# Kernel optimization log

Hardware: AMD Instinct MI355X
Metric: run time of the kernel (lower is better)

## Reference

```python
import jax, jax.numpy as jnp
import numpy as np

B, N, F_IN, F_OUT = 16, 1024, 128, 128
LEAKY_SLOPE = 0.01  # torch nn.LeakyReLU default


def setup_inputs() -> dict:
    key = jax.random.key(0)
    k1, k2, k3, k4 = jax.random.split(key, 4)
    node_mat = jax.random.normal(k1, (B, N, F_IN), dtype=jnp.float32)
    adj_mat = jax.random.uniform(k2, (B, N, N), dtype=jnp.float32)
    # nn.Linear(node_in_len, node_out_len): weight [F_OUT, F_IN], bias [F_OUT]
    bound = 1.0 / np.sqrt(F_IN)
    W = jax.random.uniform(k3, (F_OUT, F_IN), minval=-bound, maxval=bound, dtype=jnp.float32)
    b = jax.random.uniform(k4, (F_OUT,), minval=-bound, maxval=bound, dtype=jnp.float32)
    return {"node_mat": node_mat, "adj_mat": adj_mat, "W": W, "b": b}


def reference(node_mat, adj_mat, W, b):
    # degree normalization: row-scale adjacency by 1/degree
    # (the torch code builds a diagonal inv-degree matrix and bmm's it;
    #  mathematically identical to a broadcast row scale)
    n_neighbors = adj_mat.sum(axis=-1, keepdims=True)          # [B, N, 1]
    norm_adj = adj_mat / n_neighbors                           # [B, N, N]
    node_fea = jnp.einsum('bnm,bmf->bnf', norm_adj, node_mat)  # [B, N, F_in]
    node_fea = jnp.einsum('bnf,of->bno', node_fea, W) + b      # linear
    return jnp.where(node_fea >= 0, node_fea, LEAKY_SLOPE * node_fea)
```

## Files before the change

kernel.cpp:

```cpp
#include <hip/hip_runtime.h>
#include <hip/hip_bf16.h>


typedef __attribute__((ext_vector_type(8))) __bf16 bf16x8;
typedef __attribute__((ext_vector_type(4))) float f32x4;

__device__ __forceinline__ unsigned f2bf_pk(float lo, float hi) {
    union { float f; unsigned u; } a, b;
    a.f = lo; b.f = hi;
    unsigned ra = (a.u + 0x7FFFu + ((a.u >> 16) & 1u)) >> 16;
    unsigned rb = (b.u + 0x7FFFu + ((b.u >> 16) & 1u)) & 0xFFFF0000u;
    return ra | rb;
}

__device__ __forceinline__ bf16x8 cvt8(const f32x4& a, const f32x4& b) {
    union { unsigned u[4]; bf16x8 v; } r;
    r.u[0] = f2bf_pk(a.x, a.y);
    r.u[1] = f2bf_pk(a.z, a.w);
    r.u[2] = f2bf_pk(b.x, b.y);
    r.u[3] = f2bf_pk(b.z, b.w);
    return r.v;
}

__global__ __launch_bounds__(256, 2)
void k1_xw(const float* __restrict__ x, const float* __restrict__ W,
           unsigned short* __restrict__ yF)
{
    __shared__ unsigned short Ax[64 * 128];
    __shared__ unsigned short Bw[128 * 128];

    const int t   = threadIdx.x;
    const int bid = blockIdx.x;
    const int xcd = bid & 7;
    const int j   = bid >> 3;
    const int b   = xcd * 2 + (j >> 4);
    const int m0  = (j & 15) << 6;
    const float* xb = x + (((long)b << 10) + m0) * 128;

#pragma unroll
    for (int i = 0; i < 8; ++i) {
        int e = i * 1024 + t * 4;
        int r = e >> 7, f = e & 127;
        f32x4 v = *(const f32x4*)(xb + (long)r * 128 + f);
        int c = f >> 3;
        int byte = r * 256 + (((c ^ (r & 7)) << 4) | ((f & 7) << 1));
        uint2 pk; pk.x = f2bf_pk(v.x, v.y); pk.y = f2bf_pk(v.z, v.w);
        *(uint2*)((char*)Ax + byte) = pk;
    }
#pragma unroll
    for (int i = 0; i < 16; ++i) {
        int e = i * 1024 + t * 4;
        int r = e >> 7, f = e & 127;
        f32x4 v = *(const f32x4*)(W + r * 128 + f);
        int c = f >> 3;
        int byte = r * 256 + (((c ^ (r & 7)) << 4) | ((f & 7) << 1));
        uint2 pk; pk.x = f2bf_pk(v.x, v.y); pk.y = f2bf_pk(v.z, v.w);
        *(uint2*)((char*)Bw + byte) = pk;
    }
    __syncthreads();

    const int lane = t & 63, w = t >> 6;
    const int lrow = lane & 15, lq = lane >> 4;

    bf16x8 af[4];
#pragma unroll
    for (int kk = 0; kk < 4; ++kk) {
        int r = w * 16 + lrow;
        int c = kk * 4 + lq;
        af[kk] = *(const bf16x8*)((const char*)Ax + r * 256 + ((c ^ (r & 7)) << 4));
    }

    f32x4 zero = {0.f, 0.f, 0.f, 0.f};
    f32x4 acc[8] = {zero, zero, zero, zero, zero, zero, zero, zero};
#pragma unroll
    for (int nf = 0; nf < 8; ++nf) {
#pragma unroll
        for (int kk = 0; kk < 4; ++kk) {
            int o = nf * 16 + lrow;
            int c = kk * 4 + lq;
            bf16x8 bfrag = *(const bf16x8*)((const char*)Bw + o * 256 + ((c ^ (o & 7)) << 4));
            acc[nf] = __builtin_amdgcn_mfma_f32_16x16x32_bf16(af[kk], bfrag, acc[nf], 0, 0, 0);
        }
    }

    {
        const int ks = (m0 >> 5) + (w >> 1);
        const int q  = (w & 1) * 2 + (lq >> 1);
        const int jb = (lq & 1) * 4;
#pragma unroll
        for (int nf = 0; nf < 8; ++nf) {
            uint2 pk;
            pk.x = f2bf_pk(acc[nf][0], acc[nf][1]);
            pk.y = f2bf_pk(acc[nf][2], acc[nf][3]);
            long off = (((long)((b * 32 + ks) * 8 + nf)) << 9) + (q * 16 + lrow) * 8 + jb;
            *(uint2*)(yF + off) = pk;
        }
    }
}

__global__ __launch_bounds__(256, 1)
void k2_agg(const float* __restrict__ adj, const unsigned short* __restrict__ yF,
            const float* __restrict__ bias, float* __restrict__ out)
{
    __shared__ float accbuf[4][128 * 68];
    __shared__ float degw[4][64];

    const int bid = blockIdx.x;
    const int xcd = bid & 7;
    const int j   = bid >> 3;
    const int b   = xcd * 2 + (j >> 4);
    const int n0  = (j & 15) << 6;

    const int t = threadIdx.x;
    const int lane = t & 63, w = t >> 6;
    const int lrow = lane & 15, lq = lane >> 4;

    const float* adjr = adj + ((long)(b * 1024 + n0 + lrow)) * 1024 + (w << 8) + lq * 8;
    const unsigned short* fr = yF + (((long)(b * 32 + w * 8) * 8) << 9) + lane * 8;

    f32x4 zero = {0.f, 0.f, 0.f, 0.f};
    f32x4 acc[4][8];
#pragma unroll
    for (int rg = 0; rg < 4; ++rg)
#pragma unroll
        for (int ot = 0; ot < 8; ++ot) acc[rg][ot] = zero;
    float ds[4] = {0.f, 0.f, 0.f, 0.f};

#pragma unroll 2
    for (int kk = 0; kk < 8; ++kk) {
        f32x4 v0[4], v1[4];
#pragma unroll
        for (int rg = 0; rg < 4; ++rg) {
            v0[rg] = *(const f32x4*)(adjr + rg * 16384 + kk * 32);
            v1[rg] = *(const f32x4*)(adjr + rg * 16384 + kk * 32 + 4);
        }
        bf16x8 bb[8];
#pragma unroll
        for (int ot = 0; ot < 8; ++ot)
            bb[ot] = *(const bf16x8*)(fr + ((kk * 8 + ot) << 9));

        bf16x8 a[4];
#pragma unroll
        for (int rg = 0; rg < 4; ++rg) {
            ds[rg] += v0[rg].x + v0[rg].y + v0[rg].z + v0[rg].w
                    + v1[rg].x + v1[rg].y + v1[rg].z + v1[rg].w;
            a[rg] = cvt8(v0[rg], v1[rg]);
        }
#pragma unroll
        for (int rg = 0; rg < 4; ++rg)
#pragma unroll
            for (int ot = 0; ot < 8; ++ot)
                acc[rg][ot] = __builtin_amdgcn_mfma_f32_16x16x32_bf16(a[rg], bb[ot], acc[rg][ot], 0, 0, 0);
    }

#pragma unroll
    for (int rg = 0; rg < 4; ++rg) {
        float d = ds[rg];
        d += __shfl_xor(d, 16, 64);
        d += __shfl_xor(d, 32, 64);
        if (lq == 0) degw[w][rg * 16 + lrow] = d;
    }

#pragma unroll
    for (int rg = 0; rg < 4; ++rg)
#pragma unroll
        for (int ot = 0; ot < 8; ++ot)
            *(f32x4*)&accbuf[w][(ot * 16 + lrow) * 68 + rg * 16 + lq * 4] = acc[rg][ot];
    __syncthreads();

    {
        const int n = lane;
        const int o0 = w * 32;
        float deg = degw[0][n] + degw[1][n] + degw[2][n] + degw[3][n];
        float inv = 1.0f / deg;
        float res[32];
#pragma unroll
        for (int c = 0; c < 32; ++c) {
            float s = accbuf[0][(o0 + c) * 68 + n] + accbuf[1][(o0 + c) * 68 + n]
                    + accbuf[2][(o0 + c) * 68 + n] + accbuf[3][(o0 + c) * 68 + n];
            float v = s * inv + bias[o0 + c];
            res[c] = (v >= 0.f) ? v : 0.01f * v;
        }
        float* op = out + (((long)(b * 1024 + n0 + n)) << 7) + o0;
#pragma unroll
        for (int g = 0; g < 8; ++g) {
            f32x4 r = {res[g * 4], res[g * 4 + 1], res[g * 4 + 2], res[g * 4 + 3]};
            *(f32x4*)(op + g * 4) = r;
        }
    }
}

extern "C" void kernel_launch(void* const* d_in, const int* in_sizes, int n_in,
                              void* d_out, int out_size, void* d_ws, size_t ws_size,
                              hipStream_t stream) {
    const float* node = (const float*)d_in[0];
    const float* adj  = (const float*)d_in[1];
    const float* W    = (const float*)d_in[2];
    const float* bias = (const float*)d_in[3];
    float* out = (float*)d_out;
    unsigned short* yF = (unsigned short*)d_ws;

    k1_xw<<<dim3(256), dim3(256), 0, stream>>>(node, W, yF);
    k2_agg<<<dim3(256), dim3(256), 0, stream>>>(adj, yF, bias, out);
}
```

Measured before the change: 27.87 us.

## Split work finer: 32-row tiles in xW kernel, 8 waves per aggregation block

The X·W kernel now uses 32-row tiles across 512 blocks, with each wave computing half the output columns. The aggregation kernel runs 512 threads (8 waves), and each wave handles 32 rows instead of 64. This halves the per-wave accumulator count and raises occupancy and latency hiding on the adjacency stream. The cost is more redundant loads of W per block in k1, a dropped XCD-aware block mapping in k1, and a larger LDS footprint per block under launch_bounds(512,2).

```diff
diff --git a/kernel.cpp b/kernel.cpp
--- a/kernel.cpp
+++ b/kernel.cpp
@@ -26,19 +26,17 @@
 void k1_xw(const float* __restrict__ x, const float* __restrict__ W,
            unsigned short* __restrict__ yF)
 {
-    __shared__ unsigned short Ax[64 * 128];
+    __shared__ unsigned short Ax[32 * 128];
     __shared__ unsigned short Bw[128 * 128];
 
-    const int t   = threadIdx.x;
-    const int bid = blockIdx.x;
-    const int xcd = bid & 7;
-    const int j   = bid >> 3;
-    const int b   = xcd * 2 + (j >> 4);
-    const int m0  = (j & 15) << 6;
+    const int t  = threadIdx.x;
+    const int wg = blockIdx.x;
+    const int b  = wg >> 5;
+    const int m0 = (wg & 31) << 5;
     const float* xb = x + (((long)b << 10) + m0) * 128;
 
 #pragma unroll
-    for (int i = 0; i < 8; ++i) {
+    for (int i = 0; i < 4; ++i) {
         int e = i * 1024 + t * 4;
         int r = e >> 7, f = e & 127;
         f32x4 v = *(const f32x4*)(xb + (long)r * 128 + f);
@@ -60,23 +58,24 @@
     __syncthreads();
 
     const int lane = t & 63, w = t >> 6;
+    const int wm = w >> 1, wn = w & 1;
     const int lrow = lane & 15, lq = lane >> 4;
 
     bf16x8 af[4];
 #pragma unroll
     for (int kk = 0; kk < 4; ++kk) {
-        int r = w * 16 + lrow;
+        int r = wm * 16 + lrow;
         int c = kk * 4 + lq;
         af[kk] = *(const bf16x8*)((const char*)Ax + r * 256 + ((c ^ (r & 7)) << 4));
     }
 
     f32x4 zero = {0.f, 0.f, 0.f, 0.f};
-    f32x4 acc[8] = {zero, zero, zero, zero, zero, zero, zero, zero};
-#pragma unroll
-    for (int nf = 0; nf < 8; ++nf) {
+    f32x4 acc[4] = {zero, zero, zero, zero};
+#pragma unroll
+    for (int nf = 0; nf < 4; ++nf) {
 #pragma unroll
         for (int kk = 0; kk < 4; ++kk) {
-            int o = nf * 16 + lrow;
+            int o = wn * 64 + nf * 16 + lrow;
             int c = kk * 4 + lq;
             bf16x8 bfrag = *(const bf16x8*)((const char*)Bw + o * 256 + ((c ^ (o & 7)) << 4));
             acc[nf] = __builtin_amdgcn_mfma_f32_16x16x32_bf16(af[kk], bfrag, acc[nf], 0, 0, 0);
@@ -84,21 +83,22 @@
     }
 
     {
-        const int ks = (m0 >> 5) + (w >> 1);
-        const int q  = (w & 1) * 2 + (lq >> 1);
+        const int ks = wg & 31;
+        const int q  = wm * 2 + (lq >> 1);
         const int jb = (lq & 1) * 4;
 #pragma unroll
-        for (int nf = 0; nf < 8; ++nf) {
+        for (int nf = 0; nf < 4; ++nf) {
+            int ot = wn * 4 + nf;
             uint2 pk;
             pk.x = f2bf_pk(acc[nf][0], acc[nf][1]);
             pk.y = f2bf_pk(acc[nf][2], acc[nf][3]);
-            long off = (((long)((b * 32 + ks) * 8 + nf)) << 9) + (q * 16 + lrow) * 8 + jb;
+            long off = (((long)((b * 32 + ks) * 8 + ot)) << 9) + (q * 16 + lrow) * 8 + jb;
             *(uint2*)(yF + off) = pk;
         }
     }
 }
 
-__global__ __launch_bounds__(256, 1)
+__global__ __launch_bounds__(512, 2)
 void k2_agg(const float* __restrict__ adj, const unsigned short* __restrict__ yF,
             const float* __restrict__ bias, float* __restrict__ out)
 {
@@ -113,24 +113,25 @@
 
     const int t = threadIdx.x;
     const int lane = t & 63, w = t >> 6;
+    const int h = w >> 2, q = w & 3;
     const int lrow = lane & 15, lq = lane >> 4;
 
-    const float* adjr = adj + ((long)(b * 1024 + n0 + lrow)) * 1024 + (w << 8) + lq * 8;
-    const unsigned short* fr = yF + (((long)(b * 32 + w * 8) * 8) << 9) + lane * 8;
+    const float* adjr = adj + ((long)(b * 1024 + n0 + h * 32 + lrow)) * 1024 + (q << 8) + lq * 8;
+    const unsigned short* fr = yF + (((long)((b * 32 + q * 8) * 8)) << 9) + lane * 8;
 
     f32x4 zero = {0.f, 0.f, 0.f, 0.f};
-    f32x4 acc[4][8];
-#pragma unroll
-    for (int rg = 0; rg < 4; ++rg)
+    f32x4 acc[2][8];
+#pragma unroll
+    for (int rg = 0; rg < 2; ++rg)
 #pragma unroll
         for (int ot = 0; ot < 8; ++ot) acc[rg][ot] = zero;
-    float ds[4] = {0.f, 0.f, 0.f, 0.f};
-
-#pragma unroll 2
+    float ds[2] = {0.f, 0.f};
+
+#pragma unroll
     for (int kk = 0; kk < 8; ++kk) {
-        f32x4 v0[4], v1[4];
-#pragma unroll
-        for (int rg = 0; rg < 4; ++rg) {
+        f32x4 v0[2], v1[2];
+#pragma unroll
+        for (int rg = 0; rg < 2; ++rg) {
             v0[rg] = *(const f32x4*)(adjr + rg * 16384 + kk * 32);
             v1[rg] = *(const f32x4*)(adjr + rg * 16384 + kk * 32 + 4);
         }
@@ -139,43 +140,43 @@
         for (int ot = 0; ot < 8; ++ot)
             bb[ot] = *(const bf16x8*)(fr + ((kk * 8 + ot) << 9));
 
-        bf16x8 a[4];
-#pragma unroll
-        for (int rg = 0; rg < 4; ++rg) {
+        bf16x8 a[2];
+#pragma unroll
+        for (int rg = 0; rg < 2; ++rg) {
             ds[rg] += v0[rg].x + v0[rg].y + v0[rg].z + v0[rg].w
                     + v1[rg].x + v1[rg].y + v1[rg].z + v1[rg].w;
             a[rg] = cvt8(v0[rg], v1[rg]);
         }
 #pragma unroll
-        for (int rg = 0; rg < 4; ++rg)
+        for (int rg = 0; rg < 2; ++rg)
 #pragma unroll
             for (int ot = 0; ot < 8; ++ot)
                 acc[rg][ot] = __builtin_amdgcn_mfma_f32_16x16x32_bf16(a[rg], bb[ot], acc[rg][ot], 0, 0, 0);
     }
 
 #pragma unroll
-    for (int rg = 0; rg < 4; ++rg) {
+    for (int rg = 0; rg < 2; ++rg) {
         float d = ds[rg];
         d += __shfl_xor(d, 16, 64);
         d += __shfl_xor(d, 32, 64);
-        if (lq == 0) degw[w][rg * 16 + lrow] = d;
-    }
-
-#pragma unroll
-    for (int rg = 0; rg < 4; ++rg)
+        if (lq == 0) degw[q][h * 32 + rg * 16 + lrow] = d;
+    }
+
+#pragma unroll
+    for (int rg = 0; rg < 2; ++rg)
 #pragma unroll
         for (int ot = 0; ot < 8; ++ot)
-            *(f32x4*)&accbuf[w][(ot * 16 + lrow) * 68 + rg * 16 + lq * 4] = acc[rg][ot];
+            *(f32x4*)&accbuf[q][(ot * 16 + lrow) * 68 + h * 32 + rg * 16 + lq * 4] = acc[rg][ot];
     __syncthreads();
 
     {
         const int n = lane;
-        const int o0 = w * 32;
+        const int o0 = w * 16;
         float deg = degw[0][n] + degw[1][n] + degw[2][n] + degw[3][n];
         float inv = 1.0f / deg;
-        float res[32];
-#pragma unroll
-        for (int c = 0; c < 32; ++c) {
+        float res[16];
+#pragma unroll
+        for (int c = 0; c < 16; ++c) {
             float s = accbuf[0][(o0 + c) * 68 + n] + accbuf[1][(o0 + c) * 68 + n]
                     + accbuf[2][(o0 + c) * 68 + n] + accbuf[3][(o0 + c) * 68 + n];
             float v = s * inv + bias[o0 + c];
@@ -183,7 +184,7 @@
         }
         float* op = out + (((long)(b * 1024 + n0 + n)) << 7) + o0;
 #pragma unroll
-        for (int g = 0; g < 8; ++g) {
+        for (int g = 0; g < 4; ++g) {
             f32x4 r = {res[g * 4], res[g * 4 + 1], res[g * 4 + 2], res[g * 4 + 3]};
             *(f32x4*)(op + g * 4) = r;
         }
@@ -200,6 +201,6 @@
     float* out = (float*)d_out;
     unsigned short* yF = (unsigned short*)d_ws;
 
-    k1_xw<<<dim3(256), dim3(256), 0, stream>>>(node, W, yF);
-    k2_agg<<<dim3(256), dim3(256), 0, stream>>>(adj, yF, bias, out);
-}
+    k1_xw<<<dim3(512), dim3(256), 0, stream>>>(node, W, yF);
+    k2_agg<<<dim3(256), dim3(512), 0, stream>>>(adj, yF, bias, out);
+}
```

After: 29.42 us. 1.06x slower.

## Restructure aggregation kernel with double-buffered direct-to-LDS loads and 512-thread blocks

Applied to the files above, without the earlier changes.

Rewrites the aggregation kernel so 4 waves stream swizzled adjacency tiles and 4 waves stream projected-feature tiles straight into LDS using global_load_lds, double-buffered across 8 K-stages. Each wave then computes a 16x64 output slice from LDS, so the cross-wave split-K reduction through a large LDS accumulation buffer goes away. The aim is to overlap global loads with MFMA work and to cut the epilogue reduction. In exchange it adds a barrier per stage and writes the output with scattered scalar stores instead of vectorized ones.

```diff
diff --git a/kernel.cpp b/kernel.cpp
--- a/kernel.cpp
+++ b/kernel.cpp
@@ -4,6 +4,10 @@
 
 typedef __attribute__((ext_vector_type(8))) __bf16 bf16x8;
 typedef __attribute__((ext_vector_type(4))) float f32x4;
+
+#define GLD16(gp, lp) __builtin_amdgcn_global_load_lds( \
+    (const __attribute__((address_space(1))) unsigned int*)(gp), \
+    (__attribute__((address_space(3))) unsigned int*)(lp), 16, 0, 0)
 
 __device__ __forceinline__ unsigned f2bf_pk(float lo, float hi) {
     union { float f; unsigned u; } a, b;
@@ -98,12 +102,12 @@
     }
 }
 
-__global__ __launch_bounds__(256, 1)
+__global__ __launch_bounds__(512, 2)
 void k2_agg(const float* __restrict__ adj, const unsigned short* __restrict__ yF,
             const float* __restrict__ bias, float* __restrict__ out)
 {
-    __shared__ float accbuf[4][128 * 68];
-    __shared__ float degw[4][64];
+    __shared__ float          bufA[2][64 * 128];
+    __shared__ unsigned short bufY[2][32 * 512];
 
     const int bid = blockIdx.x;
     const int xcd = bid & 7;
@@ -113,81 +117,85 @@
 
     const int t = threadIdx.x;
     const int lane = t & 63, w = t >> 6;
+    const int h = w >> 1, oc = w & 1;
     const int lrow = lane & 15, lq = lane >> 4;
 
-    const float* adjr = adj + ((long)(b * 1024 + n0 + lrow)) * 1024 + (w << 8) + lq * 8;
-    const unsigned short* fr = yF + (((long)(b * 32 + w * 8) * 8) << 9) + lane * 8;
+    const float* adjb = adj + ((long)b << 20);
+
+    const int srow = (lane >> 5);
+    const int ssc  = lane & 31;
 
     f32x4 zero = {0.f, 0.f, 0.f, 0.f};
-    f32x4 acc[4][8];
-#pragma unroll
-    for (int rg = 0; rg < 4; ++rg)
-#pragma unroll
-        for (int ot = 0; ot < 8; ++ot) acc[rg][ot] = zero;
-    float ds[4] = {0.f, 0.f, 0.f, 0.f};
-
-#pragma unroll 2
-    for (int kk = 0; kk < 8; ++kk) {
-        f32x4 v0[4], v1[4];
-#pragma unroll
-        for (int rg = 0; rg < 4; ++rg) {
-            v0[rg] = *(const f32x4*)(adjr + rg * 16384 + kk * 32);
-            v1[rg] = *(const f32x4*)(adjr + rg * 16384 + kk * 32 + 4);
-        }
-        bf16x8 bb[8];
-#pragma unroll
-        for (int ot = 0; ot < 8; ++ot)
-            bb[ot] = *(const bf16x8*)(fr + ((kk * 8 + ot) << 9));
-
-        bf16x8 a[4];
-#pragma unroll
-        for (int rg = 0; rg < 4; ++rg) {
-            ds[rg] += v0[rg].x + v0[rg].y + v0[rg].z + v0[rg].w
-                    + v1[rg].x + v1[rg].y + v1[rg].z + v1[rg].w;
-            a[rg] = cvt8(v0[rg], v1[rg]);
-        }
-#pragma unroll
-        for (int rg = 0; rg < 4; ++rg)
-#pragma unroll
-            for (int ot = 0; ot < 8; ++ot)
-                acc[rg][ot] = __builtin_amdgcn_mfma_f32_16x16x32_bf16(a[rg], bb[ot], acc[rg][ot], 0, 0, 0);
-    }
-
-#pragma unroll
-    for (int rg = 0; rg < 4; ++rg) {
-        float d = ds[rg];
-        d += __shfl_xor(d, 16, 64);
-        d += __shfl_xor(d, 32, 64);
-        if (lq == 0) degw[w][rg * 16 + lrow] = d;
-    }
-
-#pragma unroll
-    for (int rg = 0; rg < 4; ++rg)
-#pragma unroll
-        for (int ot = 0; ot < 8; ++ot)
-            *(f32x4*)&accbuf[w][(ot * 16 + lrow) * 68 + rg * 16 + lq * 4] = acc[rg][ot];
+    f32x4 acc[4] = {zero, zero, zero, zero};
+    float dsum = 0.f;
+
+#define STAGE(BUF, S)                                                                  \
+    do {                                                                               \
+        if (w < 4) {                                                                   \
+            _Pragma("unroll")                                                          \
+            for (int i = 0; i < 8; ++i) {                                              \
+                int rl = w * 16 + 2 * i + srow;                                        \
+                const float* g = adjb + ((long)(n0 + rl) << 10) + (S) * 128            \
+                               + ((ssc ^ (rl & 7)) << 2);                              \
+                GLD16(g, &bufA[BUF][(w * 16 + 2 * i) * 128]);                          \
+            }                                                                          \
+        } else {                                                                       \
+            const int ks = w - 4;                                                      \
+            _Pragma("unroll")                                                          \
+            for (int i = 0; i < 8; ++i) {                                              \
+                const unsigned short* g = yF                                           \
+                    + (((long)((b * 32 + (S) * 4 + ks) * 8 + i)) << 9) + lane * 8;     \
+                GLD16(g, &bufY[BUF][(ks * 8 + i) << 9]);                               \
+            }                                                                          \
+        }                                                                              \
+    } while (0)
+
+    STAGE(0, 0);
     __syncthreads();
 
-    {
-        const int n = lane;
-        const int o0 = w * 32;
-        float deg = degw[0][n] + degw[1][n] + degw[2][n] + degw[3][n];
-        float inv = 1.0f / deg;
-        float res[32];
-#pragma unroll
-        for (int c = 0; c < 32; ++c) {
-            float s = accbuf[0][(o0 + c) * 68 + n] + accbuf[1][(o0 + c) * 68 + n]
-                    + accbuf[2][(o0 + c) * 68 + n] + accbuf[3][(o0 + c) * 68 + n];
-            float v = s * inv + bias[o0 + c];
-            res[c] = (v >= 0.f) ? v : 0.01f * v;
-        }
-        float* op = out + (((long)(b * 1024 + n0 + n)) << 7) + o0;
-#pragma unroll
-        for (int g = 0; g < 8; ++g) {
-            f32x4 r = {res[g * 4], res[g * 4 + 1], res[g * 4 + 2], res[g * 4 + 3]};
-            *(f32x4*)(op + g * 4) = r;
-        }
-    }
+    for (int s = 0; s < 8; ++s) {
+        const int cur = s & 1;
+        if (s < 7) STAGE(cur ^ 1, s + 1);
+
+        const int row = h * 16 + lrow;
+        const int rx  = row & 7;
+#pragma unroll
+        for (int kk = 0; kk < 4; ++kk) {
+            const int c0 = kk * 8 + lq * 2;
+            f32x4 a0 = *(const f32x4*)&bufA[cur][row * 128 + ((c0 ^ rx) << 2)];
+            f32x4 a1 = *(const f32x4*)&bufA[cur][row * 128 + (((c0 + 1) ^ rx) << 2)];
+            dsum += a0.x + a0.y + a0.z + a0.w + a1.x + a1.y + a1.z + a1.w;
+            bf16x8 a = cvt8(a0, a1);
+#pragma unroll
+            for (int n = 0; n < 4; ++n) {
+                const int ot = oc * 4 + n;
+                bf16x8 bb = *(const bf16x8*)&bufY[cur][((kk * 8 + ot) << 9) + lane * 8];
+                acc[n] = __builtin_amdgcn_mfma_f32_16x16x32_bf16(a, bb, acc[n], 0, 0, 0);
+            }
+        }
+        __syncthreads();
+    }
+
+    dsum += __shfl_xor(dsum, 16, 64);
+    dsum += __shfl_xor(dsum, 32, 64);
+    float invd[4];
+#pragma unroll
+    for (int i = 0; i < 4; ++i)
+        invd[i] = 1.0f / __shfl(dsum, lq * 4 + i, 64);
+
+#pragma unroll
+    for (int n = 0; n < 4; ++n) {
+        const int o = (oc * 4 + n) * 16 + lrow;
+        const float bv = bias[o];
+#pragma unroll
+        for (int i = 0; i < 4; ++i) {
+            const int r = n0 + h * 16 + lq * 4 + i;
+            float v = acc[n][i] * invd[i] + bv;
+            v = (v >= 0.f) ? v : 0.01f * v;
+            out[(((long)(b * 1024 + r)) << 7) + o] = v;
+        }
+    }
+#undef STAGE
 }
 
 extern "C" void kernel_launch(void* const* d_in, const int* in_sizes, int n_in,
@@ -201,5 +209,5 @@
     unsigned short* yF = (unsigned short*)d_ws;
 
     k1_xw<<<dim3(256), dim3(256), 0, stream>>>(node, W, yF);
-    k2_agg<<<dim3(256), dim3(256), 0, stream>>>(adj, yF, bias, out);
-}
+    k2_agg<<<dim3(256), dim3(512), 0, stream>>>(adj, yF, bias, out);
+}
```

Result: slower. 28.83 us (+3.4%).
